# Kernel optimization log

Hardware: AMD Instinct MI355X
Metric: run time of the kernel (lower is better)

The kernel has to match this reference:

```python
import jax, jax.numpy as jnp
import numpy as np
from jax import lax

TS = 64.0  # timestep_ in the original module


def get_spikes(x, th):
    # Integrate-and-fire with reset-by-subtraction (catCuda.getSpikes),
    # batched over all channels with per-channel thresholds.
    # x: [N,C,H,W,T], th: [C]
    thb = th[None, :, None, None]
    xT = jnp.moveaxis(x, -1, 0)  # [T,N,C,H,W]

    def step(v, xt):
        v = v + xt
        s = (v >= thb).astype(x.dtype)
        return v - s * thb, s

    _, sT = lax.scan(step, jnp.zeros_like(xT[0]), xT)
    return jnp.moveaxis(sT, 0, -1)  # [N,C,H,W,T]


def conv2d(x, w, b, pad):
    out = lax.conv_general_dilated(x, w, (1, 1), [(pad, pad), (pad, pad)],
                                   dimension_numbers=('NCHW', 'OIHW', 'NCHW'))
    return out + b[None, :, None, None]


def snn_conv(x, w, b, pad):
    # per-timestep 2D conv on [N,C,H,W,T]: fold T into batch
    N, C, H, W, T = x.shape
    xt = jnp.moveaxis(x, -1, 1).reshape(N * T, C, H, W)
    out = conv2d(xt, w, b, pad)
    Co, Ho, Wo = out.shape[1], out.shape[2], out.shape[3]
    return jnp.moveaxis(out.reshape(N, T, Co, Ho, Wo), 1, -1)


def avgpool2(y):
    N, C, H, W = y.shape
    return y.reshape(N, C, H // 2, 2, W // 2, 2).mean(axis=(3, 5))


def snn_pool(x):
    N, C, H, W, T = x.shape
    return x.reshape(N, C, H // 2, 2, W // 2, 2, T).mean(axis=(3, 5))


def tt(x5, y4, th):
    # threshold_training_snn: spikes from SNN pre-activation, quantized-clamped
    # ANN activation, and online per-channel threshold update.
    y_new = get_spikes(x5, th)
    y = jnp.clip(jnp.floor(y4 * TS) / TS, 0.0, 1.0)
    mul = x5.shape[0] * x5.shape[2] * x5.shape[3] * x5.shape[4]
    diff = (y.sum(axis=(0, 2, 3)) * TS - y_new.sum(axis=(0, 2, 3, 4))) / mul
    return y_new, y, th - 0.1 * diff


def setup_inputs():
    key = jax.random.key(0)
    ks = jax.random.split(key, 40)
    chans = [(3, 128), (128, 128), (128, 256), (256, 256), (256, 512), (512, 512), (512, 1024)]
    inp = {}
    for idx, (ci, co) in enumerate(chans):
        inp['w%ds' % (idx + 1)] = jax.random.normal(ks[2 * idx], (co, ci, 3, 3), jnp.float32) / np.float32(np.sqrt(ci * 9))
        inp['b%ds' % (idx + 1)] = jnp.zeros((co,), jnp.float32)
        inp['w%da' % (idx + 1)] = jax.random.normal(ks[2 * idx + 1], (co, ci, 3, 3), jnp.float32) / np.float32(np.sqrt(ci * 9))
        inp['b%da' % (idx + 1)] = jnp.zeros((co,), jnp.float32)
    inp['wc'] = jax.random.normal(ks[30], (100, 1024), jnp.float32) / 32.0
    inp['bc'] = jnp.zeros((100,), jnp.float32)
    inp['x'] = jax.random.uniform(ks[31], (4, 3, 32, 32, 64), jnp.float32)
    for name, c in [('threshold_pre_1', 128), ('threshold_pre_2', 128), ('threshold_pre_3', 256),
                    ('threshold_pre_4', 256), ('threshold_pre_5', 512), ('threshold_pre_6', 512),
                    ('threshold_pre_7', 1024), ('p1', 128), ('p2', 256), ('p3', 512), ('p4', 1024)]:
        inp[name] = jnp.ones((c,), jnp.float32)
    return inp


def reference(x, threshold_pre_1, threshold_pre_2, threshold_pre_3, threshold_pre_4,
              threshold_pre_5, threshold_pre_6, threshold_pre_7, p1, p2, p3, p4,
              w1s, b1s, w1a, b1a, w2s, b2s, w2a, b2a, w3s, b3s, w3a, b3a,
              w4s, b4s, w4a, b4a, w5s, b5s, w5a, b5a, w6s, b6s, w6a, b6a,
              w7s, b7s, w7a, b7a, wc, bc):
    x_ = x.sum(axis=-1) / TS
    xs, y, t1 = tt(snn_conv(x, w1s, b1s, 1), conv2d(x_, w1a, b1a, 1), threshold_pre_1)
    xs, y, t2 = tt(snn_conv(xs, w2s, b2s, 1), conv2d(y, w2a, b2a, 1), threshold_pre_2)
    xs, y, q1 = tt(snn_pool(xs), avgpool2(y), p1)
    xs, y, t3 = tt(snn_conv(xs, w3s, b3s, 1), conv2d(y, w3a, b3a, 1), threshold_pre_3)
    xs, y, t4 = tt(snn_conv(xs, w4s, b4s, 1), conv2d(y, w4a, b4a, 1), threshold_pre_4)
    xs, y, q2 = tt(snn_pool(xs), avgpool2(y), p2)
    xs, y, t5 = tt(snn_conv(xs, w5s, b5s, 1), conv2d(y, w5a, b5a, 1), threshold_pre_5)
    xs, y, t6 = tt(snn_conv(xs, w6s, b6s, 1), conv2d(y, w6a, b6a, 1), threshold_pre_6)
    xs, y, q3 = tt(snn_pool(xs), avgpool2(y), p3)
    xs, y, t7 = tt(snn_conv(xs, w7s, b7s, 0), conv2d(y, w7a, b7a, 0), threshold_pre_7)
    xs, y, q4 = tt(snn_pool(xs), avgpool2(y), p4)
    # classifier on [N,1024,1,1,T] spike trains, then sum over time / T
    logits_t = jnp.einsum('nct,oc->not', xs[:, :, 0, 0, :], wc) + bc[None, :, None]
    out = logits_t.sum(axis=-1) / TS
    return (out, t1, t2, t3, t4, t5, t6, t7, q1, q2, q3, q4)
```

## Files before the change

### kernel.cpp

```cpp
#include <hip/hip_runtime.h>
#include <cstdint>
#include <cstddef>


typedef short short8 __attribute__((ext_vector_type(8)));
typedef float floatx4 __attribute__((ext_vector_type(4)));

__device__ __forceinline__ unsigned short f2bf_rne(float f) {
  unsigned u = __float_as_uint(f);
  return (unsigned short)((u + 0x7FFFu + ((u >> 16) & 1u)) >> 16);
}
__device__ __forceinline__ float bf2f(unsigned short h) {
  return __uint_as_float((unsigned)h << 16);
}

__global__ __launch_bounds__(256) void k_wxform(const float* __restrict__ Wsrc,
                                                unsigned short* __restrict__ wt,
                                                int Ci, int Co) {
  const int nch = Ci >> 5;
  const int total = (Co >> 6) * nch * 9 * 4 * 64;
  int idx = blockIdx.x * 256 + threadIdx.x;
  if (idx >= total) return;
  int lane = idx & 63;
  int t2 = idx >> 6;
  int cg = t2 & 3;
  int t3 = t2 >> 2;
  int tap = t3 % 9;
  int t4 = t3 / 9;
  int ch = t4 % nch;
  int cot = t4 / nch;
  int co = cot * 64 + cg * 16 + (lane & 15);
  int cib = ch * 32 + (lane >> 4) * 8;
  short8 vh, vl;
  #pragma unroll
  for (int j = 0; j < 8; ++j) {
    float wv = Wsrc[((size_t)co * Ci + cib + j) * 9 + tap];
    unsigned short h = f2bf_rne(wv);
    vh[j] = (short)h;
    vl[j] = (short)f2bf_rne(wv - bf2f(h));
  }
  size_t base = ((((size_t)cot * nch + ch) * 9 + tap) * 4 + cg) * 1024 + (size_t)lane * 8;
  *(short8*)&wt[base] = vh;
  *(short8*)&wt[base + 512] = vl;
}

__global__ __launch_bounds__(256) void k_wxform1(const float* __restrict__ Wsrc,
                                                 unsigned short* __restrict__ wt) {
  int idx = blockIdx.x * 256 + threadIdx.x;
  if (idx >= 512) return;
  int lane = idx & 63, cg = (idx >> 6) & 3, cot = idx >> 8;
  int co = cot * 64 + cg * 16 + (lane & 15);
  short8 vh, vl;
  #pragma unroll
  for (int e = 0; e < 8; ++e) {
    int k = (lane >> 4) * 8 + e;
    float wv = 0.f;
    if (k < 27) { int tap = k / 3, ci = k - 3 * tap; wv = Wsrc[(co * 3 + ci) * 9 + tap]; }
    unsigned short h = f2bf_rne(wv);
    vh[e] = (short)h;
    vl[e] = (short)f2bf_rne(wv - bf2f(h));
  }
  size_t base = (size_t)cot * 4096 + cg * 1024 + (size_t)lane * 8;
  *(short8*)&wt[base] = vh;
  *(short8*)&wt[base + 512] = vl;
}

__global__ __launch_bounds__(256) void k_tpack(const float* __restrict__ x,
                                               unsigned* __restrict__ XT2) {
  int idx = blockIdx.x * 256 + threadIdx.x;
  int b = idx / 3072;
  int rem = idx - b * 3072;
  int t = b & 63, n = b >> 6;
  float f = x[((size_t)(n * 3072 + rem)) * 64 + t];
  unsigned short h = f2bf_rne(f);
  unsigned short l = f2bf_rne(f - bf2f(h));
  XT2[idx] = (unsigned)h | ((unsigned)l << 16);
}

__global__ __launch_bounds__(256) void k_xbar_pack(const float* __restrict__ x,
                                                   unsigned* __restrict__ xb) {
  int idx = blockIdx.x * 256 + threadIdx.x;
  if (idx >= 12288) return;
  const float* p = x + (size_t)idx * 64;
  float s = 0.f;
  #pragma unroll
  for (int t = 0; t < 64; ++t) s += p[t];
  s *= 0.015625f;
  unsigned short h = f2bf_rne(s);
  unsigned short l = f2bf_rne(s - bf2f(h));
  xb[idx] = (unsigned)h | ((unsigned)l << 16);
}

template <typename T, bool PAD0, int G, int KCH>
__global__ __launch_bounds__(256, 1) void k_cmfma(
    const T* __restrict__ in, const unsigned short* __restrict__ wt,
    const float* __restrict__ bs, float* __restrict__ out,
    int Ci, int Co, int W, int TRI, int tpi, int NIMG, int nImgValid,
    int nchPer, size_t osplit) {
  constexpr int MT = 4 * G * 16;
  constexpr int PPXMAX = PAD0 ? (MT / 4) * 16 : 208;
  constexpr int STR = KCH * 32 + 8;
  __shared__ unsigned short sIn[PPXMAX * STR];
  const int tid = threadIdx.x;
  const int lane = tid & 63;
  const int wv = tid >> 6;
  const int cot = blockIdx.x;
  const int mtile = blockIdx.y;
  const int kz = blockIdx.z;
  const int nch = Ci >> 5;
  const int nchA = kz * nchPer, nchB = nchA + nchPer;
  out += (size_t)kz * osplit;
  const int addBias = (kz == 0);

  int img_first, r0 = 0, PPR, PPX;
  if constexpr (PAD0) {
    img_first = mtile * (MT / 4);
    PPR = 16; PPX = (MT / 4) * 16;
  } else {
    img_first = (mtile / tpi) * NIMG;
    r0 = (mtile % tpi) * TRI;
    PPR = (TRI + 2) * (W + 2);
    PPX = NIMG * PPR;
  }
  const int TRW = TRI * W;

  int p0[G], mimg[G], mopx[G];
  #pragma unroll
  for (int g = 0; g < G; ++g) {
    int m = wv * (G * 16) + g * 16 + (lane & 15);
    int limg;
    if constexpr (PAD0) {
      limg = m >> 2;
      int o = m & 3;
      p0[g] = limg * 16 + (o >> 1) * 4 + (o & 1);
      mopx[g] = (o >> 1) * 2 + (o & 1);
    } else {
      limg = m / TRW;
      int rm = m - limg * TRW;
      int r = rm / W, c = rm - r * W;
      p0[g] = limg * PPR + r * (W + 2) + c;
      mopx[g] = (r0 + r) * W + c;
    }
    mimg[g] = img_first + limg;
  }
  int psh[9];
  #pragma unroll
  for (int t = 0; t < 9; ++t) {
    int dh = t / 3, dw = t - dh * 3;
    psh[t] = PAD0 ? (dh * 4 + dw) : (dh * (W + 2) + dw);
  }

  const int HWin = PAD0 ? 16 : W * W;
  int sgofs[2]; bool svalid[2];
  #pragma unroll
  for (int i = 0; i < 2; ++i) {
    int p = tid + i * 256;
    svalid[i] = false; sgofs[i] = 0;
    if (p < PPX) {
      int limg, gpx;
      if constexpr (PAD0) {
        limg = p >> 4; gpx = p & 15;
      } else {
        limg = p / PPR;
        int rem = p - limg * PPR;
        int pr = rem / (W + 2), pc = rem - pr * (W + 2);
        int gr = r0 + pr - 1, gc = pc - 1;
        gpx = (gr >= 0 && gr < W && gc >= 0 && gc < W) ? gr * W + gc : -1;
      }
      int img = img_first + limg;
      if (gpx >= 0 && img < nImgValid) {
        svalid[i] = true;
        sgofs[i] = img * Ci * HWin + gpx;
      }
    }
  }
  const int kb = (lane >> 4) * 8;

  floatx4 acc[4][G];
  floatx4 zero = {0.f, 0.f, 0.f, 0.f};
  #pragma unroll
  for (int cg = 0; cg < 4; ++cg)
    #pragma unroll
    for (int g = 0; g < G; ++g) acc[cg][g] = zero;

  for (int c2 = nchA; c2 < nchB; ++c2) {
    const int ci0 = c2 * (KCH * 32);
    #pragma unroll
    for (int i = 0; i < 2; ++i) {
      int p = tid + i * 256;
      if (p < PPX) {
        unsigned short* dst = &sIn[p * STR];
        if (svalid[i]) {
          const T* sp = in + sgofs[i] + (size_t)ci0 * HWin;
          #pragma unroll
          for (int j = 0; j < KCH * 4; ++j) {
            short8 v;
            #pragma unroll
            for (int e = 0; e < 8; ++e) {
              if constexpr (sizeof(T) == 1)
                v[e] = sp[(size_t)(j * 8 + e) * HWin] ? (short)0x3F80 : (short)0;
              else
                v[e] = (short)f2bf_rne(((const float*)sp)[(size_t)(j * 8 + e) * HWin]);
            }
            *(short8*)&dst[j * 8] = v;
          }
        } else {
          short8 z = {};
          #pragma unroll
          for (int j = 0; j < KCH * 4; ++j) *(short8*)&dst[j * 8] = z;
        }
      }
    }
    __syncthreads();
    const unsigned short* wbase = wt + ((size_t)(cot * nch + c2 * KCH)) * 36864 + (size_t)lane * 8;
    constexpr int ST = 9 * KCH;
    short8 A[2][8];
    #pragma unroll
    for (int f = 0; f < 8; ++f)
      A[0][f] = *(const short8*)(wbase + (f >> 1) * 1024 + (f & 1) * 512);
    #pragma unroll
    for (int st = 0; st < ST; ++st) {
      const int cur = st & 1;
      if (st + 1 < ST) {
        const int s1 = (st + 1) / 9, t1 = (st + 1) % 9;
        const unsigned short* wp = wbase + (size_t)s1 * 36864 + (size_t)t1 * 4096;
        #pragma unroll
        for (int f = 0; f < 8; ++f)
          A[cur ^ 1][f] = *(const short8*)(wp + (f >> 1) * 1024 + (f & 1) * 512);
      }
      const int s = st / 9, tap = st % 9;
      short8 b[G];
      #pragma unroll
      for (int g = 0; g < G; ++g)
        b[g] = *(const short8*)&sIn[(p0[g] + psh[tap]) * STR + s * 32 + kb];
      #pragma unroll
      for (int cg = 0; cg < 4; ++cg) {
        #pragma unroll
        for (int g = 0; g < G; ++g) {
          acc[cg][g] = __builtin_amdgcn_mfma_f32_16x16x32_bf16(A[cur][cg * 2 + 0], b[g], acc[cg][g], 0, 0, 0);
          acc[cg][g] = __builtin_amdgcn_mfma_f32_16x16x32_bf16(A[cur][cg * 2 + 1], b[g], acc[cg][g], 0, 0, 0);
        }
      }
    }
    __syncthreads();
  }
  const int HWout = PAD0 ? 4 : W * W;
  #pragma unroll
  for (int g = 0; g < G; ++g) {
    if (mimg[g] >= nImgValid) continue;
    #pragma unroll
    for (int cg = 0; cg < 4; ++cg) {
      #pragma unroll
      for (int i2 = 0; i2 < 4; ++i2) {
        int co = cot * 64 + cg * 16 + (lane >> 4) * 4 + i2;
        float bv = addBias ? bs[co] : 0.f;
        out[((size_t)mimg[g] * Co + co) * HWout + mopx[g]] = acc[cg][g][i2] + bv;
      }
    }
  }
}

__global__ __launch_bounds__(256, 1) void k_l1(const unsigned* __restrict__ xin,
                                               const unsigned short* __restrict__ wt,
                                               const float* __restrict__ bs,
                                               float* __restrict__ out,
                                               int nImgValid) {
  __shared__ unsigned short sIn[256 * 72];
  const int tid = threadIdx.x, lane = tid & 63, wv = tid >> 6;
  const int cot = blockIdx.x, mtile = blockIdx.y;
  const int img = mtile >> 2;
  const int r0 = (mtile & 3) * 8;
  {
    int m = tid;
    int r = r0 + (m >> 5), c = m & 31;
    const unsigned* ip = xin + (size_t)img * 3072;
    unsigned v[9][3];
    bool iv = (img < nImgValid);
    #pragma unroll
    for (int dh = 0; dh < 3; ++dh) {
      #pragma unroll
      for (int dw = 0; dw < 3; ++dw) {
        int rr = r + dh - 1, cc = c + dw - 1;
        bool ok = iv && rr >= 0 && rr < 32 && cc >= 0 && cc < 32;
        #pragma unroll
        for (int ci = 0; ci < 3; ++ci)
          v[dh * 3 + dw][ci] = ok ? ip[ci * 1024 + rr * 32 + cc] : 0u;
      }
    }
    #pragma unroll
    for (int j = 0; j < 4; ++j) {
      short8 vh, vl;
      #pragma unroll
      for (int e = 0; e < 8; ++e) {
        int k = j * 8 + e;
        unsigned u = (k < 27) ? v[k / 3][k - 3 * (k / 3)] : 0u;
        vh[e] = (short)(u & 0xFFFFu);
        vl[e] = (short)(u >> 16);
      }
      *(short8*)&sIn[m * 72 + j * 8] = vh;
      *(short8*)&sIn[m * 72 + 32 + j * 8] = vl;
    }
  }
  __syncthreads();
  const int kb = (lane >> 4) * 8;
  const unsigned short* wb = wt + (size_t)cot * 4096 + (size_t)lane * 8;
  short8 Af[8];
  #pragma unroll
  for (int f = 0; f < 8; ++f)
    Af[f] = *(const short8*)(wb + (f >> 1) * 1024 + (f & 1) * 512);
  floatx4 acc[4][4];
  floatx4 zero = {0.f, 0.f, 0.f, 0.f};
  #pragma unroll
  for (int cg = 0; cg < 4; ++cg)
    #pragma unroll
    for (int g = 0; g < 4; ++g) acc[cg][g] = zero;
  short8 bh[4], bl[4];
  #pragma unroll
  for (int g = 0; g < 4; ++g) {
    int m = wv * 64 + g * 16 + (lane & 15);
    bh[g] = *(const short8*)&sIn[m * 72 + kb];
    bl[g] = *(const short8*)&sIn[m * 72 + 32 + kb];
  }
  #pragma unroll
  for (int cg = 0; cg < 4; ++cg) {
    #pragma unroll
    for (int g = 0; g < 4; ++g) {
      acc[cg][g] = __builtin_amdgcn_mfma_f32_16x16x32_bf16(Af[cg * 2 + 0], bh[g], acc[cg][g], 0, 0, 0);
      acc[cg][g] = __builtin_amdgcn_mfma_f32_16x16x32_bf16(Af[cg * 2 + 0], bl[g], acc[cg][g], 0, 0, 0);
      acc[cg][g] = __builtin_amdgcn_mfma_f32_16x16x32_bf16(Af[cg * 2 + 1], bh[g], acc[cg][g], 0, 0, 0);
    }
  }
  if (img >= nImgValid) return;
  #pragma unroll
  for (int g = 0; g < 4; ++g) {
    int mbase = wv * 64 + g * 16 + (lane & 15);
    int px = (r0 + (mbase >> 5)) * 32 + (mbase & 31);
    #pragma unroll
    for (int cg = 0; cg < 4; ++cg) {
      #pragma unroll
      for (int i2 = 0; i2 < 4; ++i2) {
        int co = cot * 64 + cg * 16 + (lane >> 4) * 4 + i2;
        out[((size_t)img * 128 + co) * 1024 + px] = acc[cg][g][i2] + bs[co];
      }
    }
  }
}

__global__ __launch_bounds__(256) void k_if(const float* __restrict__ X,
                                            uint8_t* __restrict__ Sp,
                                            const float* __restrict__ th,
                                            float* __restrict__ ssum,
                                            int C, int HW,
                                            int nparts, size_t pstride) {
  const int CHW = C * HW;
  int idx = blockIdx.x * 256 + threadIdx.x;
  if (idx >= CHW) return;
  int c = idx / HW;
  const float thv = th[c];
  size_t base = (size_t)blockIdx.y * 64 * CHW + idx;
  const float* p = X + base;
  uint8_t* q = Sp + base;
  float v = 0.f, ss = 0.f;
  #pragma unroll
  for (int t = 0; t < 64; ++t) {
    const float* pt = p + (size_t)t * CHW;
    float xv = pt[0];
    for (int u = 1; u < nparts; ++u) xv += pt[(size_t)u * pstride];
    v += xv;
    float s = (v >= thv) ? 1.f : 0.f;
    v -= s * thv;
    q[(size_t)t * CHW] = (uint8_t)s;
    ss += s;
  }
  if ((HW & 63) == 0) {
    for (int off = 32; off >= 1; off >>= 1) ss += __shfl_down(ss, off);
    if ((threadIdx.x & 63) == 0) atomicAdd(&ssum[c], ss);
  } else {
    atomicAdd(&ssum[c], ss);
  }
}

__global__ __launch_bounds__(256) void k_ifpool(const uint8_t* __restrict__ Sin,
                                                uint8_t* __restrict__ Sp,
                                                const float* __restrict__ th,
                                                float* __restrict__ ssum,
                                                float* __restrict__ Sout,
                                                int C, int H) {
  const int Ho = H >> 1, HWo = Ho * Ho;
  const int CHWo = C * HWo;
  int idx = blockIdx.x * 256 + threadIdx.x;
  if (idx >= CHWo) return;
  int c = idx / HWo;
  int rem = idx - c * HWo;
  int ho = rem / Ho, wo = rem - ho * Ho;
  const float thv = th[c];
  const size_t istep = (size_t)C * H * H;
  const size_t ib = ((size_t)(blockIdx.y * 64) * C + c) * (H * H) + (2 * ho) * H + 2 * wo;
  uint8_t* q = Sp + (size_t)blockIdx.y * 64 * CHWo + idx;
  float v = 0.f, ss = 0.f;
  #pragma unroll
  for (int t = 0; t < 64; ++t) {
    const uint8_t* pp = Sin + ib + (size_t)t * istep;
    float xv = 0.25f * ((float)pp[0] + (float)pp[1] + (float)pp[H] + (float)pp[H + 1]);
    v += xv;
    float s = (v >= thv) ? 1.f : 0.f;
    v -= s * thv;
    q[(size_t)t * CHWo] = (uint8_t)s;
    ss += s;
  }
  if (Sout && HWo == 1) Sout[blockIdx.y * C + c] = ss;
  if ((HWo & 63) == 0) {
    for (int off = 32; off >= 1; off >>= 1) ss += __shfl_down(ss, off);
    if ((threadIdx.x & 63) == 0) atomicAdd(&ssum[c], ss);
  } else {
    atomicAdd(&ssum[c], ss);
  }
}

__global__ __launch_bounds__(256) void k_ttypool(const float* __restrict__ yin,
                                                 float* __restrict__ yout,
                                                 float* __restrict__ ysum,
                                                 int C, int H) {
  const int Ho = H >> 1, HWo = Ho * Ho;
  int idx = blockIdx.x * 256 + threadIdx.x;
  if (idx >= 4 * C * HWo) return;
  int rem = idx % (C * HWo);
  int c = rem / HWo;
  int r2 = rem - c * HWo;
  int ho = r2 / Ho, wo = r2 - ho * Ho;
  int img = idx / (C * HWo);
  size_t base = (((size_t)img * C + c) * H + 2 * ho) * H + 2 * wo;
  float xv = 0.25f * (yin[base] + yin[base + 1] + yin[base + H] + yin[base + H + 1]);
  float v = floorf(xv * 64.f) * 0.015625f;
  v = fminf(fmaxf(v, 0.f), 1.f);
  yout[idx] = v;
  if ((HWo & 63) == 0) {
    for (int off = 32; off >= 1; off >>= 1) v += __shfl_down(v, off);
    if ((threadIdx.x & 63) == 0) atomicAdd(&ysum[c], v);
  } else {
    atomicAdd(&ysum[c], v);
  }
}

__global__ __launch_bounds__(256) void k_tty(const float* __restrict__ y4,
                                             float* __restrict__ yout,
                                             float* __restrict__ ysum,
                                             int C, int HW,
                                             int nparts, int pstride) {
  int idx = blockIdx.x * 256 + threadIdx.x;
  if (idx >= 4 * C * HW) return;
  int rem = idx % (C * HW);
  int c = rem / HW;
  float xv = 0.f;
  for (int p = 0; p < nparts; ++p) xv += y4[idx + (size_t)p * pstride];
  float v = floorf(xv * 64.f) * 0.015625f;
  v = fminf(fmaxf(v, 0.f), 1.f);
  yout[idx] = v;
  if ((HW & 63) == 0) {
    for (int off = 32; off >= 1; off >>= 1) v += __shfl_down(v, off);
    if ((threadIdx.x & 63) == 0) atomicAdd(&ysum[c], v);
  } else {
    atomicAdd(&ysum[c], v);
  }
}

__global__ void k_thr(const float* __restrict__ thin,
                      const float* __restrict__ ssum,
                      const float* __restrict__ ysum,
                      float* __restrict__ dst, int C, float invmul) {
  int c = blockIdx.x * 256 + threadIdx.x;
  if (c >= C) return;
  float diff = (ysum[c] * 64.f - ssum[c]) * invmul;
  dst[c] = thin[c] - 0.1f * diff;
}

__global__ void k_cls(const float* __restrict__ S, const float* __restrict__ wc,
                      const float* __restrict__ bcp, float* __restrict__ out) {
  int idx = blockIdx.x * 256 + threadIdx.x;
  if (idx >= 400) return;
  int n = idx / 100, o = idx - (idx / 100) * 100;
  const float* sp = S + n * 1024;
  const float* wp = wc + o * 1024;
  float acc = 0.f;
  for (int c = 0; c < 1024; ++c) acc += wp[c] * sp[c];
  out[idx] = acc * 0.015625f + bcp[o];
}

extern "C" void kernel_launch(void* const* d_in, const int* in_sizes, int n_in,
                              void* d_out_v, int out_size, void* d_ws, size_t ws_size,
                              hipStream_t stream) {
  const float *Ws[7], *Bs[7], *Wa[7], *Ba[7];
  for (int i = 0; i < 7; ++i) {
    Ws[i] = (const float*)d_in[i * 4 + 0];
    Bs[i] = (const float*)d_in[i * 4 + 1];
    Wa[i] = (const float*)d_in[i * 4 + 2];
    Ba[i] = (const float*)d_in[i * 4 + 3];
  }
  const float* wc = (const float*)d_in[28];
  const float* bc = (const float*)d_in[29];
  const float* x  = (const float*)d_in[30];
  const float* TH[7];
  for (int i = 0; i < 7; ++i) TH[i] = (const float*)d_in[31 + i];
  const float* P[4];
  for (int i = 0; i < 4; ++i) P[i] = (const float*)d_in[38 + i];
  float* out = (float*)d_out_v;

  float* w = (float*)d_ws;
  const size_t RF = 8536064;
  float* Rb = w;
  size_t off = RF;
  float* xbar = w + off; off += 12288;
  float* yA   = w + off; off += 524288;
  float* yB   = w + off; off += 524288;
  float* y4   = w + off; off += 524288;
  float* S    = w + off; off += 4096;
  float* sums = w + off; off += 11 * 2048;
  uint8_t* SA = (uint8_t*)(w + off);
  uint8_t* SB = SA + 33554432;
  size_t total_bytes = off * sizeof(float) + (size_t)2 * 33554432;
  if (ws_size < total_bytes) return;
  unsigned short* WT = (unsigned short*)Rb;
  unsigned* XT2 = (unsigned*)SB;
  unsigned* xbar2 = (unsigned*)xbar;

  hipMemsetAsync(sums, 0, 11 * 2048 * sizeof(float), stream);
  k_tpack<<<3072, 256, 0, stream>>>(x, XT2);
  k_xbar_pack<<<48, 256, 0, stream>>>(x, xbar2);

  int stage = 0;

  {
    float* CF = Rb + 4096;
    float* ss = sums; float* ys = ss + 1024;
    k_wxform1<<<2, 256, 0, stream>>>(Ws[0], WT);
    for (int c = 0; c < 4; ++c) {
      k_l1<<<dim3(2, 256), 256, 0, stream>>>(XT2 + (size_t)c * 64 * 3072, WT, Bs[0], CF, 64);
      k_if<<<dim3(512, 1), 256, 0, stream>>>(CF, SA + (size_t)c * 64 * 131072,
                                             TH[0], ss, 128, 1024, 1, 0);
    }
    k_wxform1<<<2, 256, 0, stream>>>(Wa[0], WT);
    k_l1<<<dim3(2, 16), 256, 0, stream>>>(xbar2, WT, Ba[0], y4, 4);
    k_tty<<<2048, 256, 0, stream>>>(y4, yA, ys, 128, 1024, 1, 0);
    k_thr<<<1, 256, 0, stream>>>(TH[0], ss, ys, out + 400, 128, 1.0f / (4.f * 1024.f * 64.f));
    ++stage;
  }

  auto mfma_layer = [&](const uint8_t* inS, uint8_t* outS, const float* inY, float* outY,
                        int li, int Ci, int Co, int W, int TRI, int tpi, int NIMG,
                        int chunkImgs, int kzn, float* CF1,
                        int aTRI, int atpi, int akz,
                        const float* thin, int outoff) {
    const int HW = W * W;
    const int CHWo = Co * HW;
    const int nch = Ci >> 5;
    const int nch2 = Ci >> 6;
    float* ss = sums + stage * 2048; float* ys = ss + 1024;
    float* CF = Rb + (size_t)Co * Ci * 9;
    size_t osplit = (kzn == 2) ? (size_t)(CF1 - CF) : 0;
    int xgrid = ((Co / 64) * nch * 9 * 4 * 64 + 255) / 256;
    k_wxform<<<xgrid, 256, 0, stream>>>(Ws[li], WT, Ci, Co);
    int nchk = 256 / chunkImgs;
    int mt = (chunkImgs / NIMG) * tpi;
    for (int c = 0; c < nchk; ++c) {
      k_cmfma<uint8_t, false, 2, 2><<<dim3(Co / 64, mt, kzn), 256, 0, stream>>>(
          inS + (size_t)c * chunkImgs * Ci * HW, WT, Bs[li], CF,
          Ci, Co, W, TRI, tpi, NIMG, chunkImgs, nch2 / kzn, osplit);
      k_if<<<dim3((CHWo + 255) / 256, chunkImgs / 64), 256, 0, stream>>>(
          CF, outS + (size_t)c * chunkImgs * CHWo, thin, ss, Co, HW, kzn, osplit);
    }
    k_wxform<<<xgrid, 256, 0, stream>>>(Wa[li], WT, Ci, Co);
    int aosplit = 4 * CHWo;
    k_cmfma<float, false, 1, 2><<<dim3(Co / 64, 4 * atpi, akz), 256, 0, stream>>>(
        inY, WT, Ba[li], y4, Ci, Co, W, aTRI, atpi, 1, 4, nch2 / akz, (size_t)aosplit);
    k_tty<<<(4 * CHWo + 255) / 256, 256, 0, stream>>>(y4, outY, ys, Co, HW, akz, aosplit);
    k_thr<<<(Co + 255) / 256, 256, 0, stream>>>(thin, ss, ys, out + outoff, Co,
                                                1.0f / (4.f * HW * 64.f));
    ++stage;
  };

  auto pool_stage = [&](const uint8_t* inS, uint8_t* outS, const float* inY, float* outY,
                        int C, int H, const float* pthr, int outoff, float* Sout) {
    const int Ho = H / 2, HWo = Ho * Ho;
    const int CHWo = C * HWo;
    float* ss = sums + stage * 2048; float* ys = ss + 1024;
    k_ifpool<<<dim3((CHWo + 255) / 256, 4), 256, 0, stream>>>(inS, outS, pthr, ss, Sout, C, H);
    k_ttypool<<<(4 * CHWo + 255) / 256, 256, 0, stream>>>(inY, outY, ys, C, H);
    k_thr<<<(C + 255) / 256, 256, 0, stream>>>(pthr, ss, ys, out + outoff, C,
                                               1.0f / (4.f * HWo * 64.f));
    ++stage;
  };

  mfma_layer(SA, SB, yA, yB, 1, 128, 128, 32, 4, 8, 1, 64, 1, nullptr,
             2, 16, 1, TH[1], 528);
  pool_stage(SB, SA, yB, yA, 128, 32, P[0], 3216, nullptr);
  mfma_layer(SA, SB, yA, yB, 2, 128, 256, 16, 8, 2, 1, 64, 2,
             (float*)(SB + 16777216), 4, 4, 2, TH[2], 656);
  mfma_layer(SB, SA, yB, yA, 3, 256, 256, 16, 8, 2, 1, 64, 2,
             (float*)(SA + 16777216), 4, 4, 2, TH[3], 912);
  pool_stage(SA, SB, yA, yB, 256, 16, P[1], 3344, nullptr);
  mfma_layer(SB, SA, yB, yA, 4, 256, 512, 8, 8, 1, 2, 128, 2,
             (float*)(SA + 8388608), 8, 1, 4, TH[4], 1168);
  mfma_layer(SA, SB, yA, yB, 5, 512, 512, 8, 8, 1, 2, 128, 2,
             (float*)(SB + 8388608), 8, 1, 4, TH[5], 1680);
  pool_stage(SB, SA, yB, yA, 512, 8, P[2], 3600, nullptr);
  {
    float* ss = sums + stage * 2048; float* ys = ss + 1024;
    float* CF = (float*)(SA + 4194304);
    const size_t osplit = 1048576;
    int xgrid = (16 * 16 * 9 * 4 * 64 + 255) / 256;
    k_wxform<<<xgrid, 256, 0, stream>>>(Ws[6], WT, 512, 1024);
    k_cmfma<uint8_t, true, 2, 1><<<dim3(16, 8, 4), 256, 0, stream>>>(
        SA, WT, Bs[6], CF, 512, 1024, 4, 0, 1, 0, 256, 4, osplit);
    k_if<<<dim3(16, 4), 256, 0, stream>>>(CF, SB, TH[6], ss, 1024, 4, 4, osplit);
    k_wxform<<<xgrid, 256, 0, stream>>>(Wa[6], WT, 512, 1024);
    k_cmfma<float, true, 1, 1><<<dim3(16, 1, 8), 256, 0, stream>>>(
        yA, WT, Ba[6], y4, 512, 1024, 4, 0, 1, 0, 4, 2, 16384);
    k_tty<<<64, 256, 0, stream>>>(y4, yB, ys, 1024, 4, 8, 16384);
    k_thr<<<4, 256, 0, stream>>>(TH[6], ss, ys, out + 2192, 1024, 1.0f / 1024.f);
    ++stage;
  }
  pool_stage(SB, SA, yB, yA, 1024, 2, P[3], 4112, S);
  k_cls<<<2, 256, 0, stream>>>(S, wc, bc, out);
}
```

Before: 2.031 ms.

## Split conv MFMA warps over output channels instead of pixels

```diff
diff --git a/kernel.cpp b/kernel.cpp
--- a/kernel.cpp
+++ b/kernel.cpp
@@ -97,7 +97,7 @@
     const float* __restrict__ bs, float* __restrict__ out,
     int Ci, int Co, int W, int TRI, int tpi, int NIMG, int nImgValid,
     int nchPer, size_t osplit) {
-  constexpr int MT = 4 * G * 16;
+  constexpr int MT = G * 16;
   constexpr int PPXMAX = PAD0 ? (MT / 4) * 16 : 208;
   constexpr int STR = KCH * 32 + 8;
   __shared__ unsigned short sIn[PPXMAX * STR];
@@ -127,7 +127,7 @@
   int p0[G], mimg[G], mopx[G];
   #pragma unroll
   for (int g = 0; g < G; ++g) {
-    int m = wv * (G * 16) + g * 16 + (lane & 15);
+    int m = g * 16 + (lane & 15);
     int limg;
     if constexpr (PAD0) {
       limg = m >> 2;
@@ -176,12 +176,10 @@
   }
   const int kb = (lane >> 4) * 8;
 
-  floatx4 acc[4][G];
+  floatx4 acc[G];
   floatx4 zero = {0.f, 0.f, 0.f, 0.f};
   #pragma unroll
-  for (int cg = 0; cg < 4; ++cg)
-    #pragma unroll
-    for (int g = 0; g < G; ++g) acc[cg][g] = zero;
+  for (int g = 0; g < G; ++g) acc[g] = zero;
 
   for (int c2 = nchA; c2 < nchB; ++c2) {
     const int ci0 = c2 * (KCH * 32);
@@ -212,21 +210,20 @@
       }
     }
     __syncthreads();
-    const unsigned short* wbase = wt + ((size_t)(cot * nch + c2 * KCH)) * 36864 + (size_t)lane * 8;
+    const unsigned short* wbase = wt + ((size_t)(cot * nch + c2 * KCH)) * 36864
+                                  + (size_t)wv * 1024 + (size_t)lane * 8;
     constexpr int ST = 9 * KCH;
-    short8 A[2][8];
-    #pragma unroll
-    for (int f = 0; f < 8; ++f)
-      A[0][f] = *(const short8*)(wbase + (f >> 1) * 1024 + (f & 1) * 512);
+    short8 A[2][2];
+    A[0][0] = *(const short8*)(wbase);
+    A[0][1] = *(const short8*)(wbase + 512);
     #pragma unroll
     for (int st = 0; st < ST; ++st) {
       const int cur = st & 1;
       if (st + 1 < ST) {
         const int s1 = (st + 1) / 9, t1 = (st + 1) % 9;
         const unsigned short* wp = wbase + (size_t)s1 * 36864 + (size_t)t1 * 4096;
-        #pragma unroll
-        for (int f = 0; f < 8; ++f)
-          A[cur ^ 1][f] = *(const short8*)(wp + (f >> 1) * 1024 + (f & 1) * 512);
+        A[cur ^ 1][0] = *(const short8*)(wp);
+        A[cur ^ 1][1] = *(const short8*)(wp + 512);
       }
       const int s = st / 9, tap = st % 9;
       short8 b[G];
@@ -234,12 +231,9 @@
       for (int g = 0; g < G; ++g)
         b[g] = *(const short8*)&sIn[(p0[g] + psh[tap]) * STR + s * 32 + kb];
       #pragma unroll
-      for (int cg = 0; cg < 4; ++cg) {
-        #pragma unroll
-        for (int g = 0; g < G; ++g) {
-          acc[cg][g] = __builtin_amdgcn_mfma_f32_16x16x32_bf16(A[cur][cg * 2 + 0], b[g], acc[cg][g], 0, 0, 0);
-          acc[cg][g] = __builtin_amdgcn_mfma_f32_16x16x32_bf16(A[cur][cg * 2 + 1], b[g], acc[cg][g], 0, 0, 0);
-        }
+      for (int g = 0; g < G; ++g) {
+        acc[g] = __builtin_amdgcn_mfma_f32_16x16x32_bf16(A[cur][0], b[g], acc[g], 0, 0, 0);
+        acc[g] = __builtin_amdgcn_mfma_f32_16x16x32_bf16(A[cur][1], b[g], acc[g], 0, 0, 0);
       }
     }
     __syncthreads();
@@ -249,13 +243,10 @@
   for (int g = 0; g < G; ++g) {
     if (mimg[g] >= nImgValid) continue;
     #pragma unroll
-    for (int cg = 0; cg < 4; ++cg) {
-      #pragma unroll
-      for (int i2 = 0; i2 < 4; ++i2) {
-        int co = cot * 64 + cg * 16 + (lane >> 4) * 4 + i2;
-        float bv = addBias ? bs[co] : 0.f;
-        out[((size_t)mimg[g] * Co + co) * HWout + mopx[g]] = acc[cg][g][i2] + bv;
-      }
+    for (int i2 = 0; i2 < 4; ++i2) {
+      int co = cot * 64 + wv * 16 + (lane >> 4) * 4 + i2;
+      float bv = addBias ? bs[co] : 0.f;
+      out[((size_t)mimg[g] * Co + co) * HWout + mopx[g]] = acc[g][i2] + bv;
     }
   }
 }
@@ -553,7 +544,6 @@
     const int HW = W * W;
     const int CHWo = Co * HW;
     const int nch = Ci >> 5;
-    const int nch2 = Ci >> 6;
     float* ss = sums + stage * 2048; float* ys = ss + 1024;
     float* CF = Rb + (size_t)Co * Ci * 9;
     size_t osplit = (kzn == 2) ? (size_t)(CF1 - CF) : 0;
@@ -562,16 +552,16 @@
     int nchk = 256 / chunkImgs;
     int mt = (chunkImgs / NIMG) * tpi;
     for (int c = 0; c < nchk; ++c) {
-      k_cmfma<uint8_t, false, 2, 2><<<dim3(Co / 64, mt, kzn), 256, 0, stream>>>(
+      k_cmfma<uint8_t, false, 8, 1><<<dim3(Co / 64, mt, kzn), 256, 0, stream>>>(
           inS + (size_t)c * chunkImgs * Ci * HW, WT, Bs[li], CF,
-          Ci, Co, W, TRI, tpi, NIMG, chunkImgs, nch2 / kzn, osplit);
+          Ci, Co, W, TRI, tpi, NIMG, chunkImgs, nch / kzn, osplit);
       k_if<<<dim3((CHWo + 255) / 256, chunkImgs / 64), 256, 0, stream>>>(
           CF, outS + (size_t)c * chunkImgs * CHWo, thin, ss, Co, HW, kzn, osplit);
     }
     k_wxform<<<xgrid, 256, 0, stream>>>(Wa[li], WT, Ci, Co);
     int aosplit = 4 * CHWo;
-    k_cmfma<float, false, 1, 2><<<dim3(Co / 64, 4 * atpi, akz), 256, 0, stream>>>(
-        inY, WT, Ba[li], y4, Ci, Co, W, aTRI, atpi, 1, 4, nch2 / akz, (size_t)aosplit);
+    k_cmfma<float, false, 4, 1><<<dim3(Co / 64, 4 * atpi, akz), 256, 0, stream>>>(
+        inY, WT, Ba[li], y4, Ci, Co, W, aTRI, atpi, 1, 4, nch / akz, (size_t)aosplit);
     k_tty<<<(4 * CHWo + 255) / 256, 256, 0, stream>>>(y4, outY, ys, Co, HW, akz, aosplit);
     k_thr<<<(Co + 255) / 256, 256, 0, stream>>>(thin, ss, ys, out + outoff, Co,
                                                 1.0f / (4.f * HW * 64.f));
@@ -609,11 +599,11 @@
     const size_t osplit = 1048576;
     int xgrid = (16 * 16 * 9 * 4 * 64 + 255) / 256;
     k_wxform<<<xgrid, 256, 0, stream>>>(Ws[6], WT, 512, 1024);
-    k_cmfma<uint8_t, true, 2, 1><<<dim3(16, 8, 4), 256, 0, stream>>>(
+    k_cmfma<uint8_t, true, 8, 1><<<dim3(16, 8, 4), 256, 0, stream>>>(
         SA, WT, Bs[6], CF, 512, 1024, 4, 0, 1, 0, 256, 4, osplit);
     k_if<<<dim3(16, 4), 256, 0, stream>>>(CF, SB, TH[6], ss, 1024, 4, 4, osplit);
     k_wxform<<<xgrid, 256, 0, stream>>>(Wa[6], WT, 512, 1024);
-    k_cmfma<float, true, 1, 1><<<dim3(16, 1, 8), 256, 0, stream>>>(
+    k_cmfma<float, true, 4, 1><<<dim3(16, 1, 8), 256, 0, stream>>>(
         yA, WT, Ba[6], y4, 512, 1024, 4, 0, 1, 0, 4, 2, 16384);
     k_tty<<<64, 256, 0, stream>>>(y4, yB, ys, 1024, 4, 8, 16384);
     k_thr<<<4, 256, 0, stream>>>(TH[6], ss, ys, out + 2192, 1024, 1.0f / 1024.f);
```

Measured after the change: 1.999 ms. About the same (-1.6%).
